# Optimization experiments

Measured on AMD Instinct MI355X. Metric: run time of the kernel, lower is better.

Reference implementation:

```python
import jax, jax.numpy as jnp
import numpy as np

GRID = 8
Q = GRID * GRID


def _resize(x, hw):
    # F.interpolate(mode='bilinear', align_corners=False) == jax.image.resize bilinear (half-pixel)
    return jax.image.resize(x, (x.shape[0], x.shape[1], hw[0], hw[1]), method='bilinear')


def _transform(l1, l2, l3):
    hw = l1.shape[2:]
    return jnp.concatenate([l1, _resize(l2, hw), _resize(l3, hw)], axis=1)


def _mlp(x, w1, b1, w2, b2):
    return jax.nn.relu(x @ w1 + b1) @ w2 + b2


def setup_inputs():
    key = jax.random.key(0)
    ks = jax.random.split(key, 16)
    B = 4
    inp = {}
    shapes = {
        't0_l0': (B, 64, 128, 128), 't0_l1': (B, 256, 128, 128),
        't0_l2': (B, 256, 64, 64), 't0_l3': (B, 256, 32, 32),
        't1_l0': (B, 64, 128, 128), 't1_l1': (B, 256, 128, 128),
        't1_l2': (B, 256, 64, 64), 't1_l3': (B, 256, 32, 32),
    }
    for i, (n, s) in enumerate(shapes.items()):
        inp[n] = jax.random.normal(ks[i], s, dtype=jnp.float32)
    # init_query_bbox: (grid + 0.5) / grid_size, exactly as _init_layers
    xx, yy = jnp.meshgrid(jnp.arange(GRID), jnp.arange(GRID), indexing='ij')
    inp['query_bbox'] = (jnp.stack([xx, yy], -1).reshape(Q, 2).astype(jnp.float32) + 0.5) / GRID
    D = 256
    inp['off_w1'] = jax.random.normal(ks[8], (D, D // 2), dtype=jnp.float32) * 0.05
    inp['off_b1'] = jnp.zeros((D // 2,), jnp.float32)
    inp['off_w2'] = jax.random.normal(ks[9], (D // 2, 2), dtype=jnp.float32) * 0.05
    inp['off_b2'] = jnp.zeros((2,), jnp.float32)
    inp['sc_w1'] = jax.random.normal(ks[10], (D, D // 2), dtype=jnp.float32) * 0.05
    inp['sc_b1'] = jnp.zeros((D // 2,), jnp.float32)
    inp['sc_w2'] = jax.random.normal(ks[11], (D // 2, 1), dtype=jnp.float32) * 0.05
    inp['sc_b2'] = jnp.zeros((1,), jnp.float32)
    return inp


def reference(t0_l0, t0_l1, t0_l2, t0_l3, t1_l0, t1_l1, t1_l2, t1_l3,
              query_bbox, off_w1, off_b1, off_w2, off_b2, sc_w1, sc_b1, sc_w2, sc_b2):
    features = _transform(t0_l1, t0_l2, t0_l3)        # [B, 3C, H, W]
    features_next = _transform(t1_l1, t1_l2, t1_l3)
    B, C, H, W = features.shape
    shape = W
    w = W // GRID // 2                                 # half patch width (=8)
    qb = jnp.broadcast_to(query_bbox[None], (B, Q, 2))
    cp = (qb * shape).astype(jnp.int32)                # [B,Q,2] integer centers

    # ---- make_query_feat: batched patch gather (source uses batch-0 centers for all samples)
    mean_feat = features.mean(axis=1)                  # [B,H,W]
    cp0 = cp[0]                                        # [Q,2]
    rows = cp0[:, 0, None] - w + jnp.arange(2 * w)     # [Q,2w]
    cols = cp0[:, 1, None] - w + jnp.arange(2 * w)     # [Q,2w]
    patches = mean_feat[:, rows[:, :, None], cols[:, None, :]]  # [B,Q,2w,2w]
    D = 4 * w * w
    # source does torch.cat(list_over_q, dim=0).reshape(B, Q, -1): this interleaves
    # query/batch axes; replicate faithfully via transpose-then-reshape
    query_feat = jnp.transpose(patches.reshape(B, Q, D), (1, 0, 2)).reshape(B, Q, D)

    offset = _mlp(query_feat, off_w1, off_b1, off_w2, off_b2)   # [B,Q,2]
    scale = _mlp(query_feat, sc_w1, sc_b1, sc_w2, sc_b2)        # [B,Q,1]
    qb_new = (cp.astype(offset.dtype) + offset * w) / shape

    cps = (qb_new * shape).astype(jnp.int32)           # trunc toward zero == torch .to(int32)
    rs, cs = cps[..., 0] - w, cps[..., 1] - w          # [B,Q]
    re_, ce_ = cps[..., 0] + w, cps[..., 1] + w
    r = jnp.arange(H)
    c = jnp.arange(W)
    # torch slicing: negative start wraps to an empty slice -> require start >= 0;
    # end beyond H/W is clipped automatically by r < re_
    row_m = (r[None, None, :] >= rs[..., None]) & (r[None, None, :] < re_[..., None]) & (rs[..., None] >= 0)
    col_m = (c[None, None, :] >= cs[..., None]) & (c[None, None, :] < ce_[..., None]) & (cs[..., None] >= 0)
    cov = row_m[:, :, :, None] & col_m[:, :, None, :]  # [B,Q,H,W]
    tag = jnp.where(cov, jnp.arange(1, Q + 1)[None, :, None, None], 0)
    last = tag.max(axis=1)                             # [B,H,W]; 0 => pixel untouched
    sw = scale[..., 0]                                 # [B,Q]
    sm = jnp.take_along_axis(sw, jnp.maximum(last - 1, 0).reshape(B, -1), axis=1).reshape(B, H, W)
    scale_map = jnp.where(last > 0, sm, jnp.ones((), sw.dtype))
    return features * scale_map[:, None] + features_next
```

## Files before the change

### kernel.cpp

```cpp
#include <hip/hip_runtime.h>

#define HW1 16384
#define HW2 4096
#define HW3 1024
#define NB  4
#define NCH 256

typedef float f4 __attribute__((ext_vector_type(4)));

__device__ inline float4 f4add(float4 a, float4 b) {
    a.x += b.x; a.y += b.y; a.z += b.z; a.w += b.w; return a;
}

__device__ inline float bil(const float* m, int n, int y, int x, float scl, float off) {
    float fy = y * scl - off, fx = x * scl - off;
    float fy0 = floorf(fy), fx0 = floorf(fx);
    float wy = fy - fy0, wx = fx - fx0;
    int y0 = max((int)fy0, 0), y1 = min((int)fy0 + 1, n - 1);
    int x0 = max((int)fx0, 0), x1 = min((int)fx0 + 1, n - 1);
    float a = m[y0 * n + x0] * (1.f - wx) + m[y0 * n + x1] * wx;
    float b = m[y1 * n + x0] * (1.f - wx) + m[y1 * n + x1] * wx;
    return a * (1.f - wy) + b * wy;
}

__global__ __launch_bounds__(256) void k_sums(
    const float* __restrict__ l1, const float* __restrict__ l2, const float* __restrict__ l3,
    float* __restrict__ SUM1, float* __restrict__ S2, float* __restrict__ S3) {
    __shared__ float4 red[256];
    int t = threadIdx.x, s = t >> 5, g = t & 31;
    int blk = blockIdx.x;
    const float* src; float* dst; int hw; int gg;
    if (blk < 512) {
        gg = blk * 32 + g; int p4 = gg * 4;
        int b = p4 >> 14, off = p4 & (HW1 - 1);
        src = l1 + ((size_t)(b * NCH + s * 32)) * HW1 + off; dst = SUM1; hw = HW1;
    } else if (blk < 640) {
        gg = (blk - 512) * 32 + g; int p4 = gg * 4;
        int b = p4 >> 12, off = p4 & (HW2 - 1);
        src = l2 + ((size_t)(b * NCH + s * 32)) * HW2 + off; dst = S2; hw = HW2;
    } else {
        gg = (blk - 640) * 32 + g; int p4 = gg * 4;
        int b = p4 >> 10, off = p4 & (HW3 - 1);
        src = l3 + ((size_t)(b * NCH + s * 32)) * HW3 + off; dst = S3; hw = HW3;
    }
    float4 acc = make_float4(0.f, 0.f, 0.f, 0.f);
    #pragma unroll 8
    for (int c = 0; c < 32; ++c)
        acc = f4add(acc, *(const float4*)(src + (size_t)c * hw));
    red[t] = acc;
    __syncthreads();
    if (s < 4) red[t] = f4add(red[t], red[t + 128]);
    __syncthreads();
    if (s < 2) red[t] = f4add(red[t], red[t + 64]);
    __syncthreads();
    if (s == 0) {
        float4 r = f4add(red[t], red[t + 32]);
        ((float4*)dst)[gg] = r;
    }
}

__global__ __launch_bounds__(256) void k_query(
    const float* __restrict__ SUM1, const float* __restrict__ S2, const float* __restrict__ S3,
    const float* __restrict__ qb,
    const float* __restrict__ ow1, const float* __restrict__ ob1,
    const float* __restrict__ ow2, const float* __restrict__ ob2,
    const float* __restrict__ sw1, const float* __restrict__ sb1,
    const float* __restrict__ sw2, const float* __restrict__ sb2,
    int* __restrict__ RS, int* __restrict__ CS, float* __restrict__ SC) {
    __shared__ float feat[256];
    __shared__ float hid[256];
    __shared__ float res[3];
    int n = blockIdx.x, t = threadIdx.x;
    int b = n & 3, qp = n >> 2;
    int qi = qp >> 3, qj = qp & 7;
    {
        int i = t >> 4, j = t & 15;
        int y = 16 * qi + i, x = 16 * qj + j;
        float v = SUM1[b * HW1 + y * 128 + x];
        v += bil(S2 + b * HW2, 64, y, x, 0.5f, 0.25f);
        v += bil(S3 + b * HW3, 32, y, x, 0.25f, 0.375f);
        feat[t] = v * (1.0f / 768.0f);
    }
    __syncthreads();
    {
        int h = t & 127;
        const float* W  = (t < 128) ? ow1 : sw1;
        const float* Bv = (t < 128) ? ob1 : sb1;
        float acc = 0.f;
        #pragma unroll 8
        for (int d = 0; d < 256; ++d)
            acc = fmaf(feat[d], W[d * 128 + h], acc);
        hid[t] = fmaxf(acc + Bv[h], 0.f);
    }
    __syncthreads();
    int w = t >> 6, l = t & 63;
    if (w < 3) {
        float acc;
        if (w == 0)      acc = fmaf(hid[l], ow2[2 * l],     hid[l + 64] * ow2[2 * l + 128]);
        else if (w == 1) acc = fmaf(hid[l], ow2[2 * l + 1], hid[l + 64] * ow2[2 * l + 129]);
        else             acc = fmaf(hid[128 + l], sw2[l],   hid[192 + l] * sw2[l + 64]);
        #pragma unroll
        for (int off = 32; off; off >>= 1) acc += __shfl_down(acc, off);
        if (l == 0) res[w] = acc + (w == 0 ? ob2[0] : (w == 1 ? ob2[1] : sb2[0]));
    }
    __syncthreads();
    if (t == 0) {
        int q = n & 63;
        int cpx = (int)(qb[2 * q + 0] * 128.0f);
        int cpy = (int)(qb[2 * q + 1] * 128.0f);
        int cpsx = (int)((float)cpx + res[0] * 8.0f);
        int cpsy = (int)((float)cpy + res[1] * 8.0f);
        RS[n] = cpsx - 8;
        CS[n] = cpsy - 8;
        SC[n] = res[2];
    }
}

__global__ __launch_bounds__(256) void k_scalemap(
    const int* __restrict__ RS, const int* __restrict__ CS, const float* __restrict__ SC,
    float* __restrict__ SMAP) {
    __shared__ int rs[64], cs[64];
    __shared__ float sc[64];
    int t = threadIdx.x;
    int p = blockIdx.x * 256 + t;
    int b = p >> 14;
    if (t < 64) { rs[t] = RS[b * 64 + t]; cs[t] = CS[b * 64 + t]; sc[t] = SC[b * 64 + t]; }
    __syncthreads();
    int off = p & (HW1 - 1);
    int r = off >> 7, c = off & 127;
    float sv = 1.0f;
    for (int q = 63; q >= 0; --q) {
        int r0 = rs[q], c0 = cs[q];
        if (r0 >= 0 && c0 >= 0 && (unsigned)(r - r0) < 16u && (unsigned)(c - c0) < 16u) {
            sv = sc[q]; break;
        }
    }
    SMAP[p] = sv;
}

__global__ __launch_bounds__(256, 4) void k_up(
    const float* __restrict__ a2, const float* __restrict__ a3,
    const float* __restrict__ n2, const float* __restrict__ n3,
    const float* __restrict__ SMAP, float* __restrict__ out) {
    __shared__ float cur[4096];
    __shared__ float nxt[4096];
    int t = threadIdx.x;
    int c_local = blockIdx.x >> 2;
    int b = blockIdx.x & 3;
    const f4* s4 = (const f4*)(SMAP + b * HW1);
    const size_t obase = (size_t)(b * 768) * HW1;

    {
        const f4* s0 = (const f4*)(a2 + ((size_t)(b * 256 + c_local)) * HW2);
        const f4* s1 = (const f4*)(n2 + ((size_t)(b * 256 + c_local)) * HW2);
        f4* o4 = (f4*)(out + obase + (size_t)(256 + c_local) * HW1);
        for (int i = t; i < 1024; i += 256) {
            ((f4*)cur)[i] = s0[i];
            ((f4*)nxt)[i] = __builtin_nontemporal_load(&s1[i]);
        }
        __syncthreads();
        for (int i = t; i < 4096; i += 256) {
            int y = i >> 5, j = i & 31;
            int iy = (y - 1) >> 1;
            int y0 = max(iy, 0), y1 = min(iy + 1, 63);
            float wy = (y & 1) ? 0.25f : 0.75f;
            int cm1 = max(2 * j - 1, 0);
            int c0 = 2 * j, c1 = 2 * j + 1;
            int c2c = min(2 * j + 2, 63);
            const float* r0 = cur + y0 * 64; const float* r1 = cur + y1 * 64;
            const float* u0 = nxt + y0 * 64; const float* u1 = nxt + y1 * 64;
            float a0 = r0[cm1], a1v = r0[c0], a2v = r0[c1], a3v = r0[c2c];
            float b0 = r1[cm1], b1v = r1[c0], b2v = r1[c1], b3v = r1[c2c];
            float p0 = u0[cm1], p1 = u0[c0], p2 = u0[c1], p3 = u0[c2c];
            float q0 = u1[cm1], q1 = u1[c0], q2 = u1[c1], q3 = u1[c2c];
            float h0 = fmaf(0.25f, a0, 0.75f * a1v);
            float h1 = fmaf(0.75f, a1v, 0.25f * a2v);
            float h2 = fmaf(0.25f, a1v, 0.75f * a2v);
            float h3 = fmaf(0.75f, a2v, 0.25f * a3v);
            float g0 = fmaf(0.25f, b0, 0.75f * b1v);
            float g1 = fmaf(0.75f, b1v, 0.25f * b2v);
            float g2 = fmaf(0.25f, b1v, 0.75f * b2v);
            float g3 = fmaf(0.75f, b2v, 0.25f * b3v);
            float e0 = fmaf(0.25f, p0, 0.75f * p1);
            float e1 = fmaf(0.75f, p1, 0.25f * p2);
            float e2 = fmaf(0.25f, p1, 0.75f * p2);
            float e3 = fmaf(0.75f, p2, 0.25f * p3);
            float k0 = fmaf(0.25f, q0, 0.75f * q1);
            float k1 = fmaf(0.75f, q1, 0.25f * q2);
            float k2 = fmaf(0.25f, q1, 0.75f * q2);
            float k3 = fmaf(0.75f, q2, 0.25f * q3);
            f4 sv = s4[i];
            f4 r;
            r.x = fmaf(fmaf(g0 - h0, wy, h0), sv.x, fmaf(k0 - e0, wy, e0));
            r.y = fmaf(fmaf(g1 - h1, wy, h1), sv.y, fmaf(k1 - e1, wy, e1));
            r.z = fmaf(fmaf(g2 - h2, wy, h2), sv.z, fmaf(k2 - e2, wy, e2));
            r.w = fmaf(fmaf(g3 - h3, wy, h3), sv.w, fmaf(k3 - e3, wy, e3));
            o4[i] = r;
        }
    }

    __syncthreads();

    {
        const f4* s0 = (const f4*)(a3 + ((size_t)(b * 256 + c_local)) * HW3);
        const f4* s1 = (const f4*)(n3 + ((size_t)(b * 256 + c_local)) * HW3);
        f4* o4 = (f4*)(out + obase + (size_t)(512 + c_local) * HW1);
        for (int i = t; i < 256; i += 256) {
            ((f4*)cur)[i] = s0[i];
            ((f4*)nxt)[i] = __builtin_nontemporal_load(&s1[i]);
        }
        __syncthreads();
        for (int i = t; i < 4096; i += 256) {
            int y = i >> 5, j = i & 31;
            int iy = (y - 2) >> 2;
            int y0 = max(iy, 0), y1 = min(iy + 1, 31);
            int ym = y & 3;
            float wy = (ym < 2) ? (0.625f + 0.25f * ym) : (0.25f * ym - 0.375f);
            int cm1 = max(j - 1, 0);
            int c0 = j, c1 = min(j + 1, 31);
            const float* r0 = cur + y0 * 32; const float* r1 = cur + y1 * 32;
            const float* u0 = nxt + y0 * 32; const float* u1 = nxt + y1 * 32;
            float a0 = r0[cm1], a1v = r0[c0], a2v = r0[c1];
            float b0 = r1[cm1], b1v = r1[c0], b2v = r1[c1];
            float p0 = u0[cm1], p1 = u0[c0], p2 = u0[c1];
            float q0 = u1[cm1], q1 = u1[c0], q2 = u1[c1];
            float h0 = fmaf(0.375f, a0, 0.625f * a1v);
            float h1 = fmaf(0.125f, a0, 0.875f * a1v);
            float h2 = fmaf(0.875f, a1v, 0.125f * a2v);
            float h3 = fmaf(0.625f, a1v, 0.375f * a2v);
            float g0 = fmaf(0.375f, b0, 0.625f * b1v);
            float g1 = fmaf(0.125f, b0, 0.875f * b1v);
            float g2 = fmaf(0.875f, b1v, 0.125f * b2v);
            float g3 = fmaf(0.625f, b1v, 0.375f * b2v);
            float e0 = fmaf(0.375f, p0, 0.625f * p1);
            float e1 = fmaf(0.125f, p0, 0.875f * p1);
            float e2 = fmaf(0.875f, p1, 0.125f * p2);
            float e3 = fmaf(0.625f, p1, 0.375f * p2);
            float k0 = fmaf(0.375f, q0, 0.625f * q1);
            float k1 = fmaf(0.125f, q0, 0.875f * q1);
            float k2 = fmaf(0.875f, q1, 0.125f * q2);
            float k3 = fmaf(0.625f, q1, 0.375f * q2);
            f4 sv = s4[i];
            f4 r;
            r.x = fmaf(fmaf(g0 - h0, wy, h0), sv.x, fmaf(k0 - e0, wy, e0));
            r.y = fmaf(fmaf(g1 - h1, wy, h1), sv.y, fmaf(k1 - e1, wy, e1));
            r.z = fmaf(fmaf(g2 - h2, wy, h2), sv.z, fmaf(k2 - e2, wy, e2));
            r.w = fmaf(fmaf(g3 - h3, wy, h3), sv.w, fmaf(k3 - e3, wy, e3));
            o4[i] = r;
        }
    }
}

__global__ __launch_bounds__(256) void k_direct(
    const float* __restrict__ a1, const float* __restrict__ n1,
    const float* __restrict__ SMAP, float* __restrict__ out) {
    int t = threadIdx.x;
    int plane = blockIdx.x >> 1;
    int half  = blockIdx.x & 1;
    int b  = plane >> 8;
    int ch = plane & 255;
    const f4* f  = (const f4*)(a1 + ((size_t)(b * 256 + ch)) * HW1);
    const f4* fn = (const f4*)(n1 + ((size_t)(b * 256 + ch)) * HW1);
    const f4* s4 = (const f4*)(SMAP + b * HW1);
    f4* o4 = (f4*)(out + ((size_t)(b * 768 + ch)) * HW1);
    int base = half * 2048;
    #pragma unroll
    for (int k = 0; k < 8; ++k) {
        int i = base + k * 256 + t;
        f4 fv = f[i];
        f4 sv = s4[i];
        f4 nv = __builtin_nontemporal_load(&fn[i]);
        f4 r;
        r.x = fmaf(fv.x, sv.x, nv.x);
        r.y = fmaf(fv.y, sv.y, nv.y);
        r.z = fmaf(fv.z, sv.z, nv.z);
        r.w = fmaf(fv.w, sv.w, nv.w);
        o4[i] = r;
    }
}

extern "C" void kernel_launch(void* const* d_in, const int* in_sizes, int n_in,
                              void* d_out, int out_size, void* d_ws, size_t ws_size,
                              hipStream_t stream) {
    (void)in_sizes; (void)n_in; (void)out_size; (void)ws_size;
    const float* t0_l1 = (const float*)d_in[1];
    const float* t0_l2 = (const float*)d_in[2];
    const float* t0_l3 = (const float*)d_in[3];
    const float* t1_l1 = (const float*)d_in[5];
    const float* t1_l2 = (const float*)d_in[6];
    const float* t1_l3 = (const float*)d_in[7];
    const float* qb    = (const float*)d_in[8];
    const float* ow1   = (const float*)d_in[9];
    const float* ob1   = (const float*)d_in[10];
    const float* ow2   = (const float*)d_in[11];
    const float* ob2   = (const float*)d_in[12];
    const float* sw1   = (const float*)d_in[13];
    const float* sb1   = (const float*)d_in[14];
    const float* sw2   = (const float*)d_in[15];
    const float* sb2   = (const float*)d_in[16];

    char* ws = (char*)d_ws;
    float* SUM1 = (float*)(ws + 0);
    float* S2   = (float*)(ws + 262144);
    float* S3   = (float*)(ws + 327680);
    int*   RS   = (int*)  (ws + 344064);
    int*   CS   = (int*)  (ws + 345088);
    float* SC   = (float*)(ws + 346112);
    float* SMAP = (float*)(ws + 347136);
    float* out  = (float*)d_out;

    hipLaunchKernelGGL(k_sums, dim3(672), dim3(256), 0, stream,
                       t0_l1, t0_l2, t0_l3, SUM1, S2, S3);
    hipLaunchKernelGGL(k_query, dim3(256), dim3(256), 0, stream,
                       SUM1, S2, S3, qb, ow1, ob1, ow2, ob2, sw1, sb1, sw2, sb2, RS, CS, SC);
    hipLaunchKernelGGL(k_scalemap, dim3(256), dim3(256), 0, stream, RS, CS, SC, SMAP);
    hipLaunchKernelGGL(k_up, dim3(1024), dim3(256), 0, stream,
                       t0_l2, t0_l3, t1_l2, t1_l3, SMAP, out);
    hipLaunchKernelGGL(k_direct, dim3(2048), dim3(256), 0, stream,
                       t0_l1, t1_l1, SMAP, out);
}
```

Before: 104.6 us.

## Split channel sums into per-group partials and reorder direct/up kernel launches

The channel-sum kernel no longer reduces across eight channel groups in shared memory. Each block now streams one channel group over a contiguous 1024-pixel range and writes an 8-way partial-sum array. k_query adds the eight partials when it gathers features, including inside the bilinear taps, which makes its loads eight times more scattered. The launch order also changes so k_direct runs before k_up, which may help the t0_l1 data stay cached after the sums pass.

New measurement: 105.2 us. About the same (+0.6%).

```diff
diff --git a/kernel.cpp b/kernel.cpp
--- a/kernel.cpp
+++ b/kernel.cpp
@@ -8,59 +8,53 @@
 
 typedef float f4 __attribute__((ext_vector_type(4)));
 
-__device__ inline float4 f4add(float4 a, float4 b) {
-    a.x += b.x; a.y += b.y; a.z += b.z; a.w += b.w; return a;
-}
-
-__device__ inline float bil(const float* m, int n, int y, int x, float scl, float off) {
+__device__ inline float psum8(const float* __restrict__ P, int stride, int idx) {
+    float s = 0.f;
+    #pragma unroll
+    for (int g = 0; g < 8; ++g) s += P[(size_t)g * stride + idx];
+    return s;
+}
+
+__device__ inline float bilp(const float* __restrict__ P, int stride, int n,
+                             int y, int x, float scl, float off) {
     float fy = y * scl - off, fx = x * scl - off;
     float fy0 = floorf(fy), fx0 = floorf(fx);
     float wy = fy - fy0, wx = fx - fx0;
     int y0 = max((int)fy0, 0), y1 = min((int)fy0 + 1, n - 1);
     int x0 = max((int)fx0, 0), x1 = min((int)fx0 + 1, n - 1);
-    float a = m[y0 * n + x0] * (1.f - wx) + m[y0 * n + x1] * wx;
-    float b = m[y1 * n + x0] * (1.f - wx) + m[y1 * n + x1] * wx;
+    float m00 = psum8(P, stride, y0 * n + x0), m01 = psum8(P, stride, y0 * n + x1);
+    float m10 = psum8(P, stride, y1 * n + x0), m11 = psum8(P, stride, y1 * n + x1);
+    float a = m00 * (1.f - wx) + m01 * wx;
+    float b = m10 * (1.f - wx) + m11 * wx;
     return a * (1.f - wy) + b * wy;
 }
 
-__global__ __launch_bounds__(256) void k_sums(
+__global__ __launch_bounds__(256) void k_sumsA(
     const float* __restrict__ l1, const float* __restrict__ l2, const float* __restrict__ l3,
-    float* __restrict__ SUM1, float* __restrict__ S2, float* __restrict__ S3) {
-    __shared__ float4 red[256];
-    int t = threadIdx.x, s = t >> 5, g = t & 31;
-    int blk = blockIdx.x;
-    const float* src; float* dst; int hw; int gg;
+    float* __restrict__ P1, float* __restrict__ P2, float* __restrict__ P3) {
+    int t = threadIdx.x, blk = blockIdx.x;
+    const float* src; float* dst; int hw, px0, b, cg;
     if (blk < 512) {
-        gg = blk * 32 + g; int p4 = gg * 4;
-        int b = p4 >> 14, off = p4 & (HW1 - 1);
-        src = l1 + ((size_t)(b * NCH + s * 32)) * HW1 + off; dst = SUM1; hw = HW1;
+        b = blk >> 7; cg = (blk >> 4) & 7; int q = blk & 15;
+        hw = HW1; src = l1; dst = P1; px0 = q * 1024;
     } else if (blk < 640) {
-        gg = (blk - 512) * 32 + g; int p4 = gg * 4;
-        int b = p4 >> 12, off = p4 & (HW2 - 1);
-        src = l2 + ((size_t)(b * NCH + s * 32)) * HW2 + off; dst = S2; hw = HW2;
+        int k = blk - 512; b = k >> 5; cg = (k >> 2) & 7; int q = k & 3;
+        hw = HW2; src = l2; dst = P2; px0 = q * 1024;
     } else {
-        gg = (blk - 640) * 32 + g; int p4 = gg * 4;
-        int b = p4 >> 10, off = p4 & (HW3 - 1);
-        src = l3 + ((size_t)(b * NCH + s * 32)) * HW3 + off; dst = S3; hw = HW3;
-    }
-    float4 acc = make_float4(0.f, 0.f, 0.f, 0.f);
+        int k = blk - 640; b = k >> 3; cg = k & 7;
+        hw = HW3; src = l3; dst = P3; px0 = 0;
+    }
+    const f4* s = (const f4*)(src + ((size_t)(b * NCH + cg * 32)) * hw + px0);
+    int hw4 = hw >> 2;
+    f4 acc = {0.f, 0.f, 0.f, 0.f};
     #pragma unroll 8
     for (int c = 0; c < 32; ++c)
-        acc = f4add(acc, *(const float4*)(src + (size_t)c * hw));
-    red[t] = acc;
-    __syncthreads();
-    if (s < 4) red[t] = f4add(red[t], red[t + 128]);
-    __syncthreads();
-    if (s < 2) red[t] = f4add(red[t], red[t + 64]);
-    __syncthreads();
-    if (s == 0) {
-        float4 r = f4add(red[t], red[t + 32]);
-        ((float4*)dst)[gg] = r;
-    }
+        acc += s[(size_t)c * hw4 + t];
+    ((f4*)(dst + ((size_t)(b * 8 + cg)) * hw + px0))[t] = acc;
 }
 
 __global__ __launch_bounds__(256) void k_query(
-    const float* __restrict__ SUM1, const float* __restrict__ S2, const float* __restrict__ S3,
+    const float* __restrict__ P1, const float* __restrict__ P2, const float* __restrict__ P3,
     const float* __restrict__ qb,
     const float* __restrict__ ow1, const float* __restrict__ ob1,
     const float* __restrict__ ow2, const float* __restrict__ ob2,
@@ -76,9 +70,12 @@
     {
         int i = t >> 4, j = t & 15;
         int y = 16 * qi + i, x = 16 * qj + j;
-        float v = SUM1[b * HW1 + y * 128 + x];
-        v += bil(S2 + b * HW2, 64, y, x, 0.5f, 0.25f);
-        v += bil(S3 + b * HW3, 32, y, x, 0.25f, 0.375f);
+        const float* P1b = P1 + (size_t)b * 8 * HW1;
+        const float* P2b = P2 + (size_t)b * 8 * HW2;
+        const float* P3b = P3 + (size_t)b * 8 * HW3;
+        float v = psum8(P1b, HW1, y * 128 + x);
+        v += bilp(P2b, HW2, 64, y, x, 0.5f, 0.25f);
+        v += bilp(P3b, HW3, 32, y, x, 0.25f, 0.375f);
         feat[t] = v * (1.0f / 768.0f);
     }
     __syncthreads();
@@ -136,6 +133,34 @@
         }
     }
     SMAP[p] = sv;
+}
+
+__global__ __launch_bounds__(256) void k_direct(
+    const float* __restrict__ a1, const float* __restrict__ n1,
+    const float* __restrict__ SMAP, float* __restrict__ out) {
+    int t = threadIdx.x;
+    int plane = blockIdx.x >> 1;
+    int half  = blockIdx.x & 1;
+    int b  = plane >> 8;
+    int ch = plane & 255;
+    const f4* f  = (const f4*)(a1 + ((size_t)(b * 256 + ch)) * HW1);
+    const f4* fn = (const f4*)(n1 + ((size_t)(b * 256 + ch)) * HW1);
+    const f4* s4 = (const f4*)(SMAP + b * HW1);
+    f4* o4 = (f4*)(out + ((size_t)(b * 768 + ch)) * HW1);
+    int base = half * 2048;
+    #pragma unroll
+    for (int k = 0; k < 8; ++k) {
+        int i = base + k * 256 + t;
+        f4 fv = f[i];
+        f4 sv = s4[i];
+        f4 nv = __builtin_nontemporal_load(&fn[i]);
+        f4 r;
+        r.x = fmaf(fv.x, sv.x, nv.x);
+        r.y = fmaf(fv.y, sv.y, nv.y);
+        r.z = fmaf(fv.z, sv.z, nv.z);
+        r.w = fmaf(fv.w, sv.w, nv.w);
+        o4[i] = r;
+    }
 }
 
 __global__ __launch_bounds__(256, 4) void k_up(
@@ -251,34 +276,6 @@
     }
 }
 
-__global__ __launch_bounds__(256) void k_direct(
-    const float* __restrict__ a1, const float* __restrict__ n1,
-    const float* __restrict__ SMAP, float* __restrict__ out) {
-    int t = threadIdx.x;
-    int plane = blockIdx.x >> 1;
-    int half  = blockIdx.x & 1;
-    int b  = plane >> 8;
-    int ch = plane & 255;
-    const f4* f  = (const f4*)(a1 + ((size_t)(b * 256 + ch)) * HW1);
-    const f4* fn = (const f4*)(n1 + ((size_t)(b * 256 + ch)) * HW1);
-    const f4* s4 = (const f4*)(SMAP + b * HW1);
-    f4* o4 = (f4*)(out + ((size_t)(b * 768 + ch)) * HW1);
-    int base = half * 2048;
-    #pragma unroll
-    for (int k = 0; k < 8; ++k) {
-        int i = base + k * 256 + t;
-        f4 fv = f[i];
-        f4 sv = s4[i];
-        f4 nv = __builtin_nontemporal_load(&fn[i]);
-        f4 r;
-        r.x = fmaf(fv.x, sv.x, nv.x);
-        r.y = fmaf(fv.y, sv.y, nv.y);
-        r.z = fmaf(fv.z, sv.z, nv.z);
-        r.w = fmaf(fv.w, sv.w, nv.w);
-        o4[i] = r;
-    }
-}
-
 extern "C" void kernel_launch(void* const* d_in, const int* in_sizes, int n_in,
                               void* d_out, int out_size, void* d_ws, size_t ws_size,
                               hipStream_t stream) {
@@ -300,22 +297,22 @@
     const float* sb2   = (const float*)d_in[16];
 
     char* ws = (char*)d_ws;
-    float* SUM1 = (float*)(ws + 0);
-    float* S2   = (float*)(ws + 262144);
-    float* S3   = (float*)(ws + 327680);
-    int*   RS   = (int*)  (ws + 344064);
-    int*   CS   = (int*)  (ws + 345088);
-    float* SC   = (float*)(ws + 346112);
-    float* SMAP = (float*)(ws + 347136);
+    float* P1   = (float*)(ws + 0);
+    float* P2   = (float*)(ws + 2097152);
+    float* P3   = (float*)(ws + 2621440);
+    int*   RS   = (int*)  (ws + 2752512);
+    int*   CS   = (int*)  (ws + 2753536);
+    float* SC   = (float*)(ws + 2754560);
+    float* SMAP = (float*)(ws + 2755584);
     float* out  = (float*)d_out;
 
-    hipLaunchKernelGGL(k_sums, dim3(672), dim3(256), 0, stream,
-                       t0_l1, t0_l2, t0_l3, SUM1, S2, S3);
+    hipLaunchKernelGGL(k_sumsA, dim3(672), dim3(256), 0, stream,
+                       t0_l1, t0_l2, t0_l3, P1, P2, P3);
     hipLaunchKernelGGL(k_query, dim3(256), dim3(256), 0, stream,
-                       SUM1, S2, S3, qb, ow1, ob1, ow2, ob2, sw1, sb1, sw2, sb2, RS, CS, SC);
+                       P1, P2, P3, qb, ow1, ob1, ow2, ob2, sw1, sb1, sw2, sb2, RS, CS, SC);
     hipLaunchKernelGGL(k_scalemap, dim3(256), dim3(256), 0, stream, RS, CS, SC, SMAP);
+    hipLaunchKernelGGL(k_direct, dim3(2048), dim3(256), 0, stream,
+                       t0_l1, t1_l1, SMAP, out);
     hipLaunchKernelGGL(k_up, dim3(1024), dim3(256), 0, stream,
                        t0_l2, t0_l3, t1_l2, t1_l3, SMAP, out);
-    hipLaunchKernelGGL(k_direct, dim3(2048), dim3(256), 0, stream,
-                       t0_l1, t1_l1, SMAP, out);
-}
+}
```
